# Kernel tuning notes

Hardware: AMD Instinct MI355X
Metric: run time of the kernel (lower is better)

Reference implementation:

```python
import jax, jax.numpy as jnp
import numpy as np

EPS = 1e-5

def layernorm(x, g, b):
    mu = jnp.mean(x, axis=-1, keepdims=True)
    var = jnp.mean(jnp.square(x - mu), axis=-1, keepdims=True)
    return (x - mu) * jax.lax.rsqrt(var + EPS) * g + b

def setup_inputs() -> dict:
    key = jax.random.key(0)
    B, C, W = 1, 256, 64           # C = x_h_dim = query_dim
    D = 256                        # inner_dim = heads(1) * dim_head(256)
    ks = jax.random.split(key, 32)
    sc = 0.02
    inp = {
        'x': jax.random.normal(ks[0], (B, C, W, W), jnp.float32),
        'h': jax.random.normal(ks[1], (B, C, W, W), jnp.float32),
        's': jax.random.normal(ks[2], (B, C, W, W), jnp.float32),
        'm': jax.random.normal(ks[3], (B, C, W, W), jnp.float32),
        't': jax.random.normal(ks[4], (B, C), jnp.float32),
        'wt': jax.random.normal(ks[5], (C, D), jnp.float32) * sc,
        'bt': jnp.zeros((D,), jnp.float32),
        'wk_x': jax.random.normal(ks[6], (C, D), jnp.float32) * sc,
        'wv_x': jax.random.normal(ks[7], (C, D), jnp.float32) * sc,
        'g_x': jnp.ones((C,), jnp.float32), 'be_x': jnp.zeros((C,), jnp.float32),
        'wk_h': jax.random.normal(ks[8], (C, D), jnp.float32) * sc,
        'wv_h': jax.random.normal(ks[9], (C, D), jnp.float32) * sc,
        'g_h': jnp.ones((C,), jnp.float32), 'be_h': jnp.zeros((C,), jnp.float32),
        'wk_s': jax.random.normal(ks[10], (C, D), jnp.float32) * sc,
        'wv_s': jax.random.normal(ks[11], (C, D), jnp.float32) * sc,
        'g_s': jnp.ones((C,), jnp.float32), 'be_s': jnp.zeros((C,), jnp.float32),
        'wk_m': jax.random.normal(ks[12], (C, D), jnp.float32) * sc,
        'wv_m': jax.random.normal(ks[13], (C, D), jnp.float32) * sc,
        'g_m': jnp.ones((C,), jnp.float32), 'be_m': jnp.zeros((C,), jnp.float32),
        'w_geglu': jax.random.normal(ks[14], (D, 2 * D), jnp.float32) * sc,
        'b_geglu': jnp.zeros((2 * D,), jnp.float32),
        'w_ff2': jax.random.normal(ks[15], (D, D), jnp.float32) * sc,
        'b_ff2': jnp.zeros((D,), jnp.float32),
        'g_res': jnp.ones((D,), jnp.float32), 'be_res': jnp.zeros((D,), jnp.float32),
        'w_out': jax.random.normal(ks[16], (D, C), jnp.float32) * sc,
        'b_out': jnp.zeros((C,), jnp.float32),
        'imageWidth': W,
    }
    return inp

def reference(x, h, s, m, t, wt, bt, wk_x, wv_x, g_x, be_x, wk_h, wv_h, g_h, be_h,
              wk_s, wv_s, g_s, be_s, wk_m, wv_m, g_m, be_m,
              w_geglu, b_geglu, w_ff2, b_ff2, g_res, be_res, w_out, b_out, imageWidth):
    B, C, W, _ = x.shape
    N = W * W
    D = wt.shape[1]
    scale = 1.0 / jnp.sqrt(jnp.float32(D))  # dim_head**-0.5 (heads=1)

    # query: t_transform(t) broadcast over all spatial positions -> [B, N, D]
    q = t @ wt + bt
    query = jnp.broadcast_to(q[:, None, :], (B, N, D))

    def tokens(a):  # b c h w -> b (h w) c
        return a.reshape(B, C, N).transpose(0, 2, 1)

    mods = []
    for a, g, be, wk, wv in ((x, g_x, be_x, wk_x, wv_x), (h, g_h, be_h, wk_h, wv_h),
                             (s, g_s, be_s, wk_s, wv_s), (m, g_m, be_m, wk_m, wv_m)):
        a = layernorm(tokens(a), g, be)
        mods.append((a @ wk, a @ wv))  # (k, v) each [B, N, D]

    sims = [jnp.einsum('bid,bjd->bij', query, k) * scale for k, _ in mods]
    combined = jnp.concatenate(sims, axis=-1)          # [B, N, 4N]
    attn = jax.nn.softmax(combined, axis=-1)
    parts = jnp.split(attn, 4, axis=-1)

    out = sum(jnp.einsum('bij,bjd->bid', a, v) for a, (_, v) in zip(parts, mods))

    # FeedForward(inner_dim, mult=1, glu=True) on layernormed sum
    r = layernorm(out, g_res, be_res)
    gg = r @ w_geglu + b_geglu
    u, gate = jnp.split(gg, 2, axis=-1)
    ff = (u * jax.nn.gelu(gate, approximate=False)) @ w_ff2 + b_ff2

    y = ff @ w_out + b_out                              # [B, N, C]
    return y.transpose(0, 2, 1).reshape(B, C, W, W)
```

## Files before the change

### kernel.cpp

```cpp
#include <hip/hip_runtime.h>
#include <math.h>

#define N_TOK 4096

#define OFF_Q     0
#define OFF_GU    256
#define OFF_GUBU  1280
#define OFF_SIM   2048
#define OFF_MU    18432
#define OFF_RINV  34816
#define OFF_BLK   51200
#define OFF_SOFT  51248
#define OFF_W     51264
#define OFF_OUTV  52288
#define OFF_R     52544
#define OFF_GG    52800
#define OFF_FF    53312
#define OFF_Y     53568

__global__ void kInit(const float* __restrict__ bt, const float* __restrict__ b_geglu,
                      const float* __restrict__ b_ff2, const float* __restrict__ b_out,
                      float* __restrict__ ws) {
  const int tid = threadIdx.x;
  ws[OFF_GG + tid] = b_geglu[tid];
  if (tid < 256) {
    ws[OFF_Q + tid] = bt[tid];
    ws[OFF_OUTV + tid] = 0.0f;
    ws[OFF_FF + tid] = b_ff2[tid];
    ws[OFF_Y + tid] = b_out[tid];
  }
  if (tid < 8) ws[OFF_GUBU + tid] = 0.0f;
}

__global__ void kQ(const float* __restrict__ t, const float* __restrict__ wt,
                   float* __restrict__ ws) {
  const int tid = threadIdx.x;
  const int c0 = blockIdx.x * 16;
  float acc = 0.f;
  #pragma unroll
  for (int i = 0; i < 16; ++i) {
    int c = c0 + i;
    acc += t[c] * wt[c * 256 + tid];
  }
  atomicAdd(&ws[OFF_Q + tid], acc);
}

__global__ void kU(const float* __restrict__ wk0, const float* __restrict__ wk1,
                   const float* __restrict__ wk2, const float* __restrict__ wk3,
                   const float* __restrict__ g0, const float* __restrict__ g1,
                   const float* __restrict__ g2, const float* __restrict__ g3,
                   const float* __restrict__ be0, const float* __restrict__ be1,
                   const float* __restrict__ be2, const float* __restrict__ be3,
                   float* __restrict__ ws) {
  const int b = blockIdx.x;
  const int m = b >> 3;
  const int c0 = (b & 7) * 32;
  const int tid = threadIdx.x;
  const int w = tid >> 6, lane = tid & 63;
  const float* wk = (m == 0) ? wk0 : (m == 1) ? wk1 : (m == 2) ? wk2 : wk3;
  const float* g  = (m == 0) ? g0  : (m == 1) ? g1  : (m == 2) ? g2  : g3;
  const float* be = (m == 0) ? be0 : (m == 1) ? be1 : (m == 2) ? be2 : be3;

  __shared__ float qsh[256];
  __shared__ float red[8];
  qsh[tid] = ws[OFF_Q + tid];
  __syncthreads();
  const float4 qv = ((const float4*)qsh)[lane];

  float lGU = 0.f, lBU = 0.f;
  #pragma unroll
  for (int r = 0; r < 8; ++r) {
    int c = c0 + w * 8 + r;
    float4 w4 = ((const float4*)(wk + c * 256))[lane];
    float s = w4.x * qv.x + w4.y * qv.y + w4.z * qv.z + w4.w * qv.w;
    for (int o = 32; o > 0; o >>= 1) s += __shfl_down(s, o, 64);
    if (lane == 0) {
      float u = s;
      float gu = g[c] * u;
      ws[OFF_GU + m * 256 + c] = gu;
      lGU += gu;
      lBU += be[c] * u;
    }
  }
  if (lane == 0) { red[w] = lGU; red[4 + w] = lBU; }
  __syncthreads();
  if (tid == 0) {
    atomicAdd(&ws[OFF_GUBU + m], red[0] + red[1] + red[2] + red[3]);
    atomicAdd(&ws[OFF_GUBU + 4 + m], red[4] + red[5] + red[6] + red[7]);
  }
}

__global__ void kB(const float* __restrict__ A0, const float* __restrict__ A1,
                   const float* __restrict__ A2, const float* __restrict__ A3,
                   float* __restrict__ ws) {
  const int b = blockIdx.x;
  const int m = b >> 6;
  const int jbase = (b & 63) * 64;
  const int tid = threadIdx.x;
  const int l = tid & 63;
  const int qq = tid >> 6;
  const float* A = (m == 0) ? A0 : (m == 1) ? A1 : (m == 2) ? A2 : A3;

  __shared__ float gu[256];
  __shared__ float p1[256], p2[256], p3[256];
  gu[tid] = ws[OFF_GU + m * 256 + tid];
  __syncthreads();

  float s1 = 0.f, s2 = 0.f, s3 = 0.f;
  const float* Abase = A + jbase + l;
  #pragma unroll 8
  for (int i = 0; i < 64; ++i) {
    int c = qq * 64 + i;
    float v = Abase[c * N_TOK];
    s1 += v;
    s2 += v * v;
    s3 += v * gu[c];
  }
  p1[tid] = s1; p2[tid] = s2; p3[tid] = s3;
  __syncthreads();
  if (tid < 64) {
    float S1 = p1[tid] + p1[tid + 64] + p1[tid + 128] + p1[tid + 192];
    float S2 = p2[tid] + p2[tid + 64] + p2[tid + 128] + p2[tid + 192];
    float S3 = p3[tid] + p3[tid + 64] + p3[tid + 128] + p3[tid + 192];
    float mu   = S1 * (1.0f / 256.0f);
    float var  = S2 * (1.0f / 256.0f) - mu * mu;
    float rinv = rsqrtf(var + 1e-5f);
    float GU = ws[OFF_GUBU + m];
    float BU = ws[OFF_GUBU + 4 + m];
    float sim = 0.0625f * (rinv * (S3 - mu * GU) + BU);
    int gj = m * N_TOK + jbase + tid;
    ws[OFF_SIM + gj] = sim;
    ws[OFF_MU + gj] = mu;
    ws[OFF_RINV + gj] = rinv;
  }
}

__global__ void kC1(float* __restrict__ ws) {
  const int b = blockIdx.x;
  const int tid = threadIdx.x;
  const int base = b * 1024;
  __shared__ float sred[4];

  float v[4];
  float mx = -1e30f;
  #pragma unroll
  for (int i = 0; i < 4; ++i) {
    v[i] = ws[OFF_SIM + base + i * 256 + tid];
    mx = fmaxf(mx, v[i]);
  }
  for (int o = 32; o > 0; o >>= 1) mx = fmaxf(mx, __shfl_down(mx, o, 64));
  if ((tid & 63) == 0) sred[tid >> 6] = mx;
  __syncthreads();
  const float mxb = fmaxf(fmaxf(sred[0], sred[1]), fmaxf(sred[2], sred[3]));
  __syncthreads();

  float se = 0.f, srm = 0.f;
  #pragma unroll
  for (int i = 0; i < 4; ++i) {
    int idx = base + i * 256 + tid;
    float e = expf(v[i] - mxb);
    se += e;
    srm += e * ws[OFF_RINV + idx] * ws[OFF_MU + idx];
  }
  for (int o = 32; o > 0; o >>= 1) se += __shfl_down(se, o, 64);
  if ((tid & 63) == 0) sred[tid >> 6] = se;
  __syncthreads();
  float seT = sred[0] + sred[1] + sred[2] + sred[3];
  __syncthreads();
  for (int o = 32; o > 0; o >>= 1) srm += __shfl_down(srm, o, 64);
  if ((tid & 63) == 0) sred[tid >> 6] = srm;
  __syncthreads();
  if (tid == 0) {
    float srmT = sred[0] + sred[1] + sred[2] + sred[3];
    ws[OFF_BLK + b * 3 + 0] = mxb;
    ws[OFF_BLK + b * 3 + 1] = seT;
    ws[OFF_BLK + b * 3 + 2] = srmT;
  }
}

__global__ void kC2(float* __restrict__ ws) {
  if (threadIdx.x != 0) return;
  float mx[16], se[16], srm[16];
  float M = -1e30f;
  for (int b = 0; b < 16; ++b) {
    mx[b] = ws[OFF_BLK + b * 3 + 0];
    se[b] = ws[OFF_BLK + b * 3 + 1];
    srm[b] = ws[OFF_BLK + b * 3 + 2];
    M = fmaxf(M, mx[b]);
  }
  float S = 0.f, As[4] = {0, 0, 0, 0}, P[4] = {0, 0, 0, 0};
  for (int b = 0; b < 16; ++b) {
    float f = expf(mx[b] - M);
    int m = b >> 2;
    S += se[b] * f;
    As[m] += se[b] * f;
    P[m] += srm[b] * f;
  }
  float inv = 1.0f / S;
  ws[OFF_SOFT + 0] = M;
  ws[OFF_SOFT + 1] = inv;
  for (int m = 0; m < 4; ++m) {
    ws[OFF_SOFT + 2 + m] = As[m] * inv;
    ws[OFF_SOFT + 6 + m] = P[m] * inv;
  }
}

__global__ void kD(const float* __restrict__ A0, const float* __restrict__ A1,
                   const float* __restrict__ A2, const float* __restrict__ A3,
                   const float* __restrict__ g0, const float* __restrict__ g1,
                   const float* __restrict__ g2, const float* __restrict__ g3,
                   const float* __restrict__ be0, const float* __restrict__ be1,
                   const float* __restrict__ be2, const float* __restrict__ be3,
                   float* __restrict__ ws) {
  const int b = blockIdx.x;
  const int m = b >> 8;
  const int c = b & 255;
  const int tid = threadIdx.x;
  const float* A = (m == 0) ? A0 : (m == 1) ? A1 : (m == 2) ? A2 : A3;
  const float* row = A + c * N_TOK;
  const float M = ws[OFF_SOFT + 0];
  const float inv = ws[OFF_SOFT + 1];

  float s = 0.f;
  #pragma unroll 4
  for (int i = 0; i < 16; ++i) {
    int j = i * 256 + tid;
    int gj = m * N_TOK + j;
    float a = expf(ws[OFF_SIM + gj] - M) * ws[OFF_RINV + gj];
    s += a * row[j];
  }
  __shared__ float red[4];
  for (int o = 32; o > 0; o >>= 1) s += __shfl_down(s, o, 64);
  if ((tid & 63) == 0) red[tid >> 6] = s;
  __syncthreads();
  if (tid == 0) {
    float dot = (red[0] + red[1] + red[2] + red[3]) * inv;
    const float* g  = (m == 0) ? g0  : (m == 1) ? g1  : (m == 2) ? g2  : g3;
    const float* be = (m == 0) ? be0 : (m == 1) ? be1 : (m == 2) ? be2 : be3;
    float P  = ws[OFF_SOFT + 6 + m];
    float As = ws[OFF_SOFT + 2 + m];
    ws[OFF_W + m * 256 + c] = g[c] * (dot - P) + be[c] * As;
  }
}

__global__ void kE(const float* __restrict__ wv0, const float* __restrict__ wv1,
                   const float* __restrict__ wv2, const float* __restrict__ wv3,
                   float* __restrict__ ws) {
  const int b = blockIdx.x;
  const int m = b >> 2;
  const int cbase = (b & 3) * 64;
  const int d = threadIdx.x;
  const float* wv = (m == 0) ? wv0 : (m == 1) ? wv1 : (m == 2) ? wv2 : wv3;
  float s = 0.f;
  #pragma unroll 8
  for (int i = 0; i < 64; ++i) {
    int c = cbase + i;
    s += ws[OFF_W + m * 256 + c] * wv[c * 256 + d];
  }
  atomicAdd(&ws[OFF_OUTV + d], s);
}

__global__ void kT1(const float* __restrict__ g_res, const float* __restrict__ be_res,
                    float* __restrict__ ws) {
  const int tid = threadIdx.x;
  __shared__ float red[4];
  float od = ws[OFF_OUTV + tid];
  float s = od;
  for (int o = 32; o > 0; o >>= 1) s += __shfl_down(s, o, 64);
  if ((tid & 63) == 0) red[tid >> 6] = s;
  __syncthreads();
  float mu = (red[0] + red[1] + red[2] + red[3]) * (1.0f / 256.0f);
  __syncthreads();
  float dv = od - mu;
  s = dv * dv;
  for (int o = 32; o > 0; o >>= 1) s += __shfl_down(s, o, 64);
  if ((tid & 63) == 0) red[tid >> 6] = s;
  __syncthreads();
  float var = (red[0] + red[1] + red[2] + red[3]) * (1.0f / 256.0f);
  ws[OFF_R + tid] = dv * rsqrtf(var + 1e-5f) * g_res[tid] + be_res[tid];
}

__global__ void kT2(const float* __restrict__ w_geglu, float* __restrict__ ws) {
  const int b = blockIdx.x;
  const int dt = b >> 4;
  const int d0 = (b & 15) * 16;
  const int tid = threadIdx.x;
  float acc = 0.f;
  #pragma unroll
  for (int i = 0; i < 16; ++i) {
    int d = d0 + i;
    acc += ws[OFF_R + d] * w_geglu[d * 512 + dt * 256 + tid];
  }
  atomicAdd(&ws[OFF_GG + dt * 256 + tid], acc);
}

__global__ void kT3(const float* __restrict__ w_ff2, float* __restrict__ ws) {
  const int c0 = blockIdx.x * 16;
  const int tid = threadIdx.x;
  float acc = 0.f;
  #pragma unroll
  for (int i = 0; i < 16; ++i) {
    int c = c0 + i;
    float u = ws[OFF_GG + c];
    float gate = ws[OFF_GG + 256 + c];
    float f = u * 0.5f * gate * (1.0f + erff(gate * 0.70710678118654752f));
    acc += f * w_ff2[c * 256 + tid];
  }
  atomicAdd(&ws[OFF_FF + tid], acc);
}

__global__ void kT4(const float* __restrict__ w_out, float* __restrict__ ws) {
  const int d0 = blockIdx.x * 16;
  const int tid = threadIdx.x;
  float acc = 0.f;
  #pragma unroll
  for (int i = 0; i < 16; ++i) {
    int d = d0 + i;
    acc += ws[OFF_FF + d] * w_out[d * 256 + tid];
  }
  atomicAdd(&ws[OFF_Y + tid], acc);
}

__global__ void kG(const float* __restrict__ ws, float4* __restrict__ out4) {
  const int idx = blockIdx.x * 256 + threadIdx.x;
  const int c = idx >> 10;
  float v = ws[OFF_Y + c];
  out4[idx] = make_float4(v, v, v, v);
}

extern "C" void kernel_launch(void* const* d_in, const int* in_sizes, int n_in,
                              void* d_out, int out_size, void* d_ws, size_t ws_size,
                              hipStream_t stream) {
  const float* x = (const float*)d_in[0];
  const float* h = (const float*)d_in[1];
  const float* s = (const float*)d_in[2];
  const float* m = (const float*)d_in[3];
  const float* t = (const float*)d_in[4];
  const float* wt = (const float*)d_in[5];
  const float* bt = (const float*)d_in[6];
  const float* wk_x = (const float*)d_in[7];
  const float* wv_x = (const float*)d_in[8];
  const float* g_x = (const float*)d_in[9];
  const float* be_x = (const float*)d_in[10];
  const float* wk_h = (const float*)d_in[11];
  const float* wv_h = (const float*)d_in[12];
  const float* g_h = (const float*)d_in[13];
  const float* be_h = (const float*)d_in[14];
  const float* wk_s = (const float*)d_in[15];
  const float* wv_s = (const float*)d_in[16];
  const float* g_s = (const float*)d_in[17];
  const float* be_s = (const float*)d_in[18];
  const float* wk_m = (const float*)d_in[19];
  const float* wv_m = (const float*)d_in[20];
  const float* g_m = (const float*)d_in[21];
  const float* be_m = (const float*)d_in[22];
  const float* w_geglu = (const float*)d_in[23];
  const float* b_geglu = (const float*)d_in[24];
  const float* w_ff2 = (const float*)d_in[25];
  const float* b_ff2 = (const float*)d_in[26];
  const float* g_res = (const float*)d_in[27];
  const float* be_res = (const float*)d_in[28];
  const float* w_out = (const float*)d_in[29];
  const float* b_out = (const float*)d_in[30];
  float* ws = (float*)d_ws;

  kInit<<<dim3(1), dim3(512), 0, stream>>>(bt, b_geglu, b_ff2, b_out, ws);
  kQ<<<dim3(16), dim3(256), 0, stream>>>(t, wt, ws);
  kU<<<dim3(32), dim3(256), 0, stream>>>(wk_x, wk_h, wk_s, wk_m,
      g_x, g_h, g_s, g_m, be_x, be_h, be_s, be_m, ws);
  kB<<<dim3(256), dim3(256), 0, stream>>>(x, h, s, m, ws);
  kC1<<<dim3(16), dim3(256), 0, stream>>>(ws);
  kC2<<<dim3(1), dim3(64), 0, stream>>>(ws);
  kD<<<dim3(1024), dim3(256), 0, stream>>>(x, h, s, m,
      g_x, g_h, g_s, g_m, be_x, be_h, be_s, be_m, ws);
  kE<<<dim3(16), dim3(256), 0, stream>>>(wv_x, wv_h, wv_s, wv_m, ws);
  kT1<<<dim3(1), dim3(256), 0, stream>>>(g_res, be_res, ws);
  kT2<<<dim3(32), dim3(256), 0, stream>>>(w_geglu, ws);
  kT3<<<dim3(16), dim3(256), 0, stream>>>(w_ff2, ws);
  kT4<<<dim3(16), dim3(256), 0, stream>>>(w_out, ws);
  kG<<<dim3(1024), dim3(256), 0, stream>>>(ws, (float4*)d_out);
}
```

Baseline: 168.2 us.

## Fuse all stages into one cooperative persistent kernel with grid syncs

Replaces the chain of thirteen small kernel launches with a single cooperative kernel of 512 blocks that runs every stage, separated by grid-wide barriers. The Q projection is recomputed in each of the 32 U blocks, and GU/BU partial sums are stored per block rather than accumulated atomically. The stats pass is re-tiled to use float4 loads over 32-token chunks. The aim is to remove launch gaps and per-kernel overhead on a latency-bound pipeline, at the cost of about ten grid barriers and redundant Q computation. The old multi-kernel path is kept as a fallback when the cooperative launch cannot run.

Result: slower. 670.5 us (+298.7%).

```diff
diff --git a/kernel.cpp b/kernel.cpp
--- a/kernel.cpp
+++ b/kernel.cpp
@@ -1,22 +1,322 @@
 #include <hip/hip_runtime.h>
+#include <hip/hip_cooperative_groups.h>
 #include <math.h>
 
+namespace cg = cooperative_groups;
+
 #define N_TOK 4096
 
-#define OFF_Q     0
-#define OFF_GU    256
-#define OFF_GUBU  1280
+#define OFF_GU    0
+#define OFF_GUP   1024
+#define OFF_BUP   1056
 #define OFF_SIM   2048
 #define OFF_MU    18432
 #define OFF_RINV  34816
 #define OFF_BLK   51200
-#define OFF_SOFT  51248
 #define OFF_W     51264
 #define OFF_OUTV  52288
 #define OFF_R     52544
 #define OFF_GG    52800
 #define OFF_FF    53312
 #define OFF_Y     53568
+#define OFF_Q     53824
+#define OFF_SOFT  54080
+
+struct Params {
+  const float *x, *h, *s, *m, *t, *wt, *bt;
+  const float *wk0, *wv0, *g0, *be0;
+  const float *wk1, *wv1, *g1, *be1;
+  const float *wk2, *wv2, *g2, *be2;
+  const float *wk3, *wv3, *g3, *be3;
+  const float *w_geglu, *b_geglu, *w_ff2, *b_ff2;
+  const float *g_res, *be_res, *w_out, *b_out;
+  float* ws;
+  float4* out4;
+};
+
+__global__ __launch_bounds__(256, 2) void fused(Params p) {
+  cg::grid_group grid = cg::this_grid();
+  const int gid = blockIdx.x;
+  const int tid = threadIdx.x;
+  float* ws = p.ws;
+
+  __shared__ float sh[3328];
+
+  const float* Aarr[4] = {p.x, p.h, p.s, p.m};
+  const float* garr[4] = {p.g0, p.g1, p.g2, p.g3};
+  const float* bearr[4] = {p.be0, p.be1, p.be2, p.be3};
+
+  if (gid < 32) {
+    const int m = gid >> 3;
+    const int c0 = (gid & 7) * 32;
+    const float* wkarr[4] = {p.wk0, p.wk1, p.wk2, p.wk3};
+    const float* wk = wkarr[m];
+    const float* g = garr[m];
+    const float* be = bearr[m];
+
+    float acc = p.bt[tid];
+    #pragma unroll 8
+    for (int c = 0; c < 256; ++c) acc += p.t[c] * p.wt[c * 256 + tid];
+    sh[tid] = acc;
+    __syncthreads();
+
+    const int w = tid >> 6, lane = tid & 63;
+    const float4 qv = ((const float4*)sh)[lane];
+    float lGU = 0.f, lBU = 0.f;
+    #pragma unroll
+    for (int r = 0; r < 8; ++r) {
+      int c = c0 + w * 8 + r;
+      float4 w4 = ((const float4*)(wk + c * 256))[lane];
+      float sdot = w4.x * qv.x + w4.y * qv.y + w4.z * qv.z + w4.w * qv.w;
+      for (int o = 32; o > 0; o >>= 1) sdot += __shfl_down(sdot, o, 64);
+      if (lane == 0) {
+        float u = sdot;
+        float gu = g[c] * u;
+        ws[OFF_GU + m * 256 + c] = gu;
+        lGU += gu;
+        lBU += be[c] * u;
+      }
+    }
+    __syncthreads();
+    if (lane == 0) { sh[256 + w] = lGU; sh[260 + w] = lBU; }
+    __syncthreads();
+    if (tid == 0) {
+      ws[OFF_GUP + m * 8 + (gid & 7)] = sh[256] + sh[257] + sh[258] + sh[259];
+      ws[OFF_BUP + m * 8 + (gid & 7)] = sh[260] + sh[261] + sh[262] + sh[263];
+    }
+  } else if (gid == 32) {
+    ws[OFF_OUTV + tid] = 0.0f;
+    ws[OFF_GG + tid] = p.b_geglu[tid];
+    ws[OFF_GG + 256 + tid] = p.b_geglu[256 + tid];
+    ws[OFF_FF + tid] = p.b_ff2[tid];
+    ws[OFF_Y + tid] = p.b_out[tid];
+  }
+  grid.sync();
+
+  {
+    const int m = gid >> 7;
+    const int jbase = (gid & 127) * 32;
+    const int l = tid & 7;
+    const int qg = tid >> 3;
+    const float* A = Aarr[m];
+
+    float* gu_sh = sh;
+    float* p1 = sh + 256;
+    float* p2 = sh + 1280;
+    float* p3 = sh + 2304;
+    gu_sh[tid] = ws[OFF_GU + m * 256 + tid];
+    __syncthreads();
+
+    float s1[4] = {0, 0, 0, 0}, s2[4] = {0, 0, 0, 0}, s3[4] = {0, 0, 0, 0};
+    #pragma unroll
+    for (int i = 0; i < 8; ++i) {
+      int c = qg * 8 + i;
+      float4 v4 = ((const float4*)(A + c * N_TOK + jbase))[l];
+      float gv = gu_sh[c];
+      s1[0] += v4.x; s2[0] += v4.x * v4.x; s3[0] += v4.x * gv;
+      s1[1] += v4.y; s2[1] += v4.y * v4.y; s3[1] += v4.y * gv;
+      s1[2] += v4.z; s2[2] += v4.z * v4.z; s3[2] += v4.z * gv;
+      s1[3] += v4.w; s2[3] += v4.w * v4.w; s3[3] += v4.w * gv;
+    }
+    #pragma unroll
+    for (int k = 0; k < 4; ++k) {
+      int tok = l * 4 + k;
+      p1[qg * 32 + tok] = s1[k];
+      p2[qg * 32 + tok] = s2[k];
+      p3[qg * 32 + tok] = s3[k];
+    }
+    __syncthreads();
+    if (tid < 32) {
+      float S1 = 0.f, S2 = 0.f, S3 = 0.f;
+      #pragma unroll 8
+      for (int q = 0; q < 32; ++q) {
+        S1 += p1[q * 32 + tid];
+        S2 += p2[q * 32 + tid];
+        S3 += p3[q * 32 + tid];
+      }
+      float GU = 0.f, BU = 0.f;
+      #pragma unroll
+      for (int i = 0; i < 8; ++i) {
+        GU += ws[OFF_GUP + m * 8 + i];
+        BU += ws[OFF_BUP + m * 8 + i];
+      }
+      float mu = S1 * (1.0f / 256.0f);
+      float var = S2 * (1.0f / 256.0f) - mu * mu;
+      float rinv = rsqrtf(var + 1e-5f);
+      float sim = 0.0625f * (rinv * (S3 - mu * GU) + BU);
+      int gj = m * N_TOK + jbase + tid;
+      ws[OFF_SIM + gj] = sim;
+      ws[OFF_MU + gj] = mu;
+      ws[OFF_RINV + gj] = rinv;
+    }
+  }
+  grid.sync();
+
+  if (gid < 16) {
+    const int base = gid * 1024;
+    float v[4];
+    float mx = -1e30f;
+    #pragma unroll
+    for (int i = 0; i < 4; ++i) {
+      v[i] = ws[OFF_SIM + base + i * 256 + tid];
+      mx = fmaxf(mx, v[i]);
+    }
+    for (int o = 32; o > 0; o >>= 1) mx = fmaxf(mx, __shfl_down(mx, o, 64));
+    if ((tid & 63) == 0) sh[tid >> 6] = mx;
+    __syncthreads();
+    const float mxb = fmaxf(fmaxf(sh[0], sh[1]), fmaxf(sh[2], sh[3]));
+    __syncthreads();
+    float se = 0.f, srm = 0.f;
+    #pragma unroll
+    for (int i = 0; i < 4; ++i) {
+      int idx = base + i * 256 + tid;
+      float e = expf(v[i] - mxb);
+      se += e;
+      srm += e * ws[OFF_RINV + idx] * ws[OFF_MU + idx];
+    }
+    for (int o = 32; o > 0; o >>= 1) se += __shfl_down(se, o, 64);
+    if ((tid & 63) == 0) sh[tid >> 6] = se;
+    __syncthreads();
+    float seT = sh[0] + sh[1] + sh[2] + sh[3];
+    __syncthreads();
+    for (int o = 32; o > 0; o >>= 1) srm += __shfl_down(srm, o, 64);
+    if ((tid & 63) == 0) sh[tid >> 6] = srm;
+    __syncthreads();
+    if (tid == 0) {
+      ws[OFF_BLK + gid * 3 + 0] = mxb;
+      ws[OFF_BLK + gid * 3 + 1] = seT;
+      ws[OFF_BLK + gid * 3 + 2] = sh[0] + sh[1] + sh[2] + sh[3];
+    }
+  }
+  grid.sync();
+
+  {
+    const int m = gid >> 7;
+    const int cbase = (gid & 127) * 2;
+
+    float M = -1e30f;
+    #pragma unroll
+    for (int b = 0; b < 16; ++b) M = fmaxf(M, ws[OFF_BLK + b * 3]);
+    float S = 0.f, Asm = 0.f, Pm = 0.f;
+    #pragma unroll
+    for (int b = 0; b < 16; ++b) {
+      float f = expf(ws[OFF_BLK + b * 3] - M);
+      float sef = ws[OFF_BLK + b * 3 + 1] * f;
+      S += sef;
+      if ((b >> 2) == m) {
+        Asm += sef;
+        Pm += ws[OFF_BLK + b * 3 + 2] * f;
+      }
+    }
+    const float inv = 1.0f / S;
+
+    for (int r = 0; r < 2; ++r) {
+      const int c = cbase + r;
+      const float* row = Aarr[m] + c * N_TOK;
+      float sacc = 0.f;
+      #pragma unroll 4
+      for (int i = 0; i < 16; ++i) {
+        int j = i * 256 + tid;
+        int gj = m * N_TOK + j;
+        float a = expf(ws[OFF_SIM + gj] - M) * ws[OFF_RINV + gj];
+        sacc += a * row[j];
+      }
+      for (int o = 32; o > 0; o >>= 1) sacc += __shfl_down(sacc, o, 64);
+      if ((tid & 63) == 0) sh[tid >> 6] = sacc;
+      __syncthreads();
+      if (tid == 0) {
+        float dot = (sh[0] + sh[1] + sh[2] + sh[3]) * inv;
+        ws[OFF_W + m * 256 + c] =
+            garr[m][c] * (dot - Pm * inv) + bearr[m][c] * (Asm * inv);
+      }
+      __syncthreads();
+    }
+  }
+  grid.sync();
+
+  if (gid < 16) {
+    const int m = gid >> 2;
+    const int cbase = (gid & 3) * 64;
+    const float* wvarr[4] = {p.wv0, p.wv1, p.wv2, p.wv3};
+    const float* wv = wvarr[m];
+    float sacc = 0.f;
+    #pragma unroll 8
+    for (int i = 0; i < 64; ++i) {
+      int c = cbase + i;
+      sacc += ws[OFF_W + m * 256 + c] * wv[c * 256 + tid];
+    }
+    atomicAdd(&ws[OFF_OUTV + tid], sacc);
+  }
+  grid.sync();
+
+  if (gid == 0) {
+    float od = ws[OFF_OUTV + tid];
+    float sr = od;
+    for (int o = 32; o > 0; o >>= 1) sr += __shfl_down(sr, o, 64);
+    if ((tid & 63) == 0) sh[tid >> 6] = sr;
+    __syncthreads();
+    float mu = (sh[0] + sh[1] + sh[2] + sh[3]) * (1.0f / 256.0f);
+    __syncthreads();
+    float dv = od - mu;
+    sr = dv * dv;
+    for (int o = 32; o > 0; o >>= 1) sr += __shfl_down(sr, o, 64);
+    if ((tid & 63) == 0) sh[tid >> 6] = sr;
+    __syncthreads();
+    float var = (sh[0] + sh[1] + sh[2] + sh[3]) * (1.0f / 256.0f);
+    ws[OFF_R + tid] = dv * rsqrtf(var + 1e-5f) * p.g_res[tid] + p.be_res[tid];
+  }
+  grid.sync();
+
+  if (gid < 32) {
+    const int dt = gid >> 4;
+    const int d0 = (gid & 15) * 16;
+    float acc = 0.f;
+    #pragma unroll
+    for (int i = 0; i < 16; ++i) {
+      int d = d0 + i;
+      acc += ws[OFF_R + d] * p.w_geglu[d * 512 + dt * 256 + tid];
+    }
+    atomicAdd(&ws[OFF_GG + dt * 256 + tid], acc);
+  }
+  grid.sync();
+
+  if (gid < 16) {
+    const int c0 = gid * 16;
+    float acc = 0.f;
+    #pragma unroll
+    for (int i = 0; i < 16; ++i) {
+      int c = c0 + i;
+      float u = ws[OFF_GG + c];
+      float gate = ws[OFF_GG + 256 + c];
+      float f = u * 0.5f * gate * (1.0f + erff(gate * 0.70710678118654752f));
+      acc += f * p.w_ff2[c * 256 + tid];
+    }
+    atomicAdd(&ws[OFF_FF + tid], acc);
+  }
+  grid.sync();
+
+  if (gid < 16) {
+    const int d0 = gid * 16;
+    float acc = 0.f;
+    #pragma unroll
+    for (int i = 0; i < 16; ++i) {
+      int d = d0 + i;
+      acc += ws[OFF_FF + d] * p.w_out[d * 256 + tid];
+    }
+    atomicAdd(&ws[OFF_Y + tid], acc);
+  }
+  grid.sync();
+
+  {
+    #pragma unroll
+    for (int k = 0; k < 2; ++k) {
+      const int idx = gid * 512 + k * 256 + tid;
+      const int c = idx >> 10;
+      float v = ws[OFF_Y + c];
+      p.out4[idx] = make_float4(v, v, v, v);
+    }
+  }
+}
 
 __global__ void kInit(const float* __restrict__ bt, const float* __restrict__ b_geglu,
                       const float* __restrict__ b_ff2, const float* __restrict__ b_out,
@@ -29,7 +329,8 @@
     ws[OFF_FF + tid] = b_ff2[tid];
     ws[OFF_Y + tid] = b_out[tid];
   }
-  if (tid < 8) ws[OFF_GUBU + tid] = 0.0f;
+  if (tid < 8) { ws[OFF_GUP + tid * 4] = 0.0f; }
+  if (tid < 64) { ws[OFF_GUP + tid] = 0.0f; ws[OFF_BUP] = ws[OFF_BUP]; }
 }
 
 __global__ void kQ(const float* __restrict__ t, const float* __restrict__ wt,
@@ -85,8 +386,8 @@
   if (lane == 0) { red[w] = lGU; red[4 + w] = lBU; }
   __syncthreads();
   if (tid == 0) {
-    atomicAdd(&ws[OFF_GUBU + m], red[0] + red[1] + red[2] + red[3]);
-    atomicAdd(&ws[OFF_GUBU + 4 + m], red[4] + red[5] + red[6] + red[7]);
+    ws[OFF_GUP + m * 8 + (b & 7)] = red[0] + red[1] + red[2] + red[3];
+    ws[OFF_BUP + m * 8 + (b & 7)] = red[4] + red[5] + red[6] + red[7];
   }
 }
 
@@ -122,11 +423,15 @@
     float S1 = p1[tid] + p1[tid + 64] + p1[tid + 128] + p1[tid + 192];
     float S2 = p2[tid] + p2[tid + 64] + p2[tid + 128] + p2[tid + 192];
     float S3 = p3[tid] + p3[tid + 64] + p3[tid + 128] + p3[tid + 192];
+    float GU = 0.f, BU = 0.f;
+    #pragma unroll
+    for (int i = 0; i < 8; ++i) {
+      GU += ws[OFF_GUP + m * 8 + i];
+      BU += ws[OFF_BUP + m * 8 + i];
+    }
     float mu   = S1 * (1.0f / 256.0f);
     float var  = S2 * (1.0f / 256.0f) - mu * mu;
     float rinv = rsqrtf(var + 1e-5f);
-    float GU = ws[OFF_GUBU + m];
-    float BU = ws[OFF_GUBU + 4 + m];
     float sim = 0.0625f * (rinv * (S3 - mu * GU) + BU);
     int gj = m * N_TOK + jbase + tid;
     ws[OFF_SIM + gj] = sim;
@@ -171,30 +476,23 @@
   if ((tid & 63) == 0) sred[tid >> 6] = srm;
   __syncthreads();
   if (tid == 0) {
-    float srmT = sred[0] + sred[1] + sred[2] + sred[3];
     ws[OFF_BLK + b * 3 + 0] = mxb;
     ws[OFF_BLK + b * 3 + 1] = seT;
-    ws[OFF_BLK + b * 3 + 2] = srmT;
+    ws[OFF_BLK + b * 3 + 2] = sred[0] + sred[1] + sred[2] + sred[3];
   }
 }
 
 __global__ void kC2(float* __restrict__ ws) {
   if (threadIdx.x != 0) return;
-  float mx[16], se[16], srm[16];
   float M = -1e30f;
-  for (int b = 0; b < 16; ++b) {
-    mx[b] = ws[OFF_BLK + b * 3 + 0];
-    se[b] = ws[OFF_BLK + b * 3 + 1];
-    srm[b] = ws[OFF_BLK + b * 3 + 2];
-    M = fmaxf(M, mx[b]);
-  }
+  for (int b = 0; b < 16; ++b) M = fmaxf(M, ws[OFF_BLK + b * 3]);
   float S = 0.f, As[4] = {0, 0, 0, 0}, P[4] = {0, 0, 0, 0};
   for (int b = 0; b < 16; ++b) {
-    float f = expf(mx[b] - M);
+    float f = expf(ws[OFF_BLK + b * 3] - M);
     int m = b >> 2;
-    S += se[b] * f;
-    As[m] += se[b] * f;
-    P[m] += srm[b] * f;
+    S += ws[OFF_BLK + b * 3 + 1] * f;
+    As[m] += ws[OFF_BLK + b * 3 + 1] * f;
+    P[m] += ws[OFF_BLK + b * 3 + 2] * f;
   }
   float inv = 1.0f / S;
   ws[OFF_SOFT + 0] = M;
@@ -237,9 +535,8 @@
     float dot = (red[0] + red[1] + red[2] + red[3]) * inv;
     const float* g  = (m == 0) ? g0  : (m == 1) ? g1  : (m == 2) ? g2  : g3;
     const float* be = (m == 0) ? be0 : (m == 1) ? be1 : (m == 2) ? be2 : be3;
-    float P  = ws[OFF_SOFT + 6 + m];
-    float As = ws[OFF_SOFT + 2 + m];
-    ws[OFF_W + m * 256 + c] = g[c] * (dot - P) + be[c] * As;
+    ws[OFF_W + m * 256 + c] =
+        g[c] * (dot - ws[OFF_SOFT + 6 + m]) + be[c] * ws[OFF_SOFT + 2 + m];
   }
 }
 
@@ -331,52 +628,67 @@
 extern "C" void kernel_launch(void* const* d_in, const int* in_sizes, int n_in,
                               void* d_out, int out_size, void* d_ws, size_t ws_size,
                               hipStream_t stream) {
-  const float* x = (const float*)d_in[0];
-  const float* h = (const float*)d_in[1];
-  const float* s = (const float*)d_in[2];
-  const float* m = (const float*)d_in[3];
-  const float* t = (const float*)d_in[4];
-  const float* wt = (const float*)d_in[5];
-  const float* bt = (const float*)d_in[6];
-  const float* wk_x = (const float*)d_in[7];
-  const float* wv_x = (const float*)d_in[8];
-  const float* g_x = (const float*)d_in[9];
-  const float* be_x = (const float*)d_in[10];
-  const float* wk_h = (const float*)d_in[11];
-  const float* wv_h = (const float*)d_in[12];
-  const float* g_h = (const float*)d_in[13];
-  const float* be_h = (const float*)d_in[14];
-  const float* wk_s = (const float*)d_in[15];
-  const float* wv_s = (const float*)d_in[16];
-  const float* g_s = (const float*)d_in[17];
-  const float* be_s = (const float*)d_in[18];
-  const float* wk_m = (const float*)d_in[19];
-  const float* wv_m = (const float*)d_in[20];
-  const float* g_m = (const float*)d_in[21];
-  const float* be_m = (const float*)d_in[22];
-  const float* w_geglu = (const float*)d_in[23];
-  const float* b_geglu = (const float*)d_in[24];
-  const float* w_ff2 = (const float*)d_in[25];
-  const float* b_ff2 = (const float*)d_in[26];
-  const float* g_res = (const float*)d_in[27];
-  const float* be_res = (const float*)d_in[28];
-  const float* w_out = (const float*)d_in[29];
-  const float* b_out = (const float*)d_in[30];
+  Params p;
+  p.x = (const float*)d_in[0];
+  p.h = (const float*)d_in[1];
+  p.s = (const float*)d_in[2];
+  p.m = (const float*)d_in[3];
+  p.t = (const float*)d_in[4];
+  p.wt = (const float*)d_in[5];
+  p.bt = (const float*)d_in[6];
+  p.wk0 = (const float*)d_in[7];
+  p.wv0 = (const float*)d_in[8];
+  p.g0 = (const float*)d_in[9];
+  p.be0 = (const float*)d_in[10];
+  p.wk1 = (const float*)d_in[11];
+  p.wv1 = (const float*)d_in[12];
+  p.g1 = (const float*)d_in[13];
+  p.be1 = (const float*)d_in[14];
+  p.wk2 = (const float*)d_in[15];
+  p.wv2 = (const float*)d_in[16];
+  p.g2 = (const float*)d_in[17];
+  p.be2 = (const float*)d_in[18];
+  p.wk3 = (const float*)d_in[19];
+  p.wv3 = (const float*)d_in[20];
+  p.g3 = (const float*)d_in[21];
+  p.be3 = (const float*)d_in[22];
+  p.w_geglu = (const float*)d_in[23];
+  p.b_geglu = (const float*)d_in[24];
+  p.w_ff2 = (const float*)d_in[25];
+  p.b_ff2 = (const float*)d_in[26];
+  p.g_res = (const float*)d_in[27];
+  p.be_res = (const float*)d_in[28];
+  p.w_out = (const float*)d_in[29];
+  p.b_out = (const float*)d_in[30];
+  p.ws = (float*)d_ws;
+  p.out4 = (float4*)d_out;
   float* ws = (float*)d_ws;
 
-  kInit<<<dim3(1), dim3(512), 0, stream>>>(bt, b_geglu, b_ff2, b_out, ws);
-  kQ<<<dim3(16), dim3(256), 0, stream>>>(t, wt, ws);
-  kU<<<dim3(32), dim3(256), 0, stream>>>(wk_x, wk_h, wk_s, wk_m,
-      g_x, g_h, g_s, g_m, be_x, be_h, be_s, be_m, ws);
-  kB<<<dim3(256), dim3(256), 0, stream>>>(x, h, s, m, ws);
+  int nb = 0;
+  hipError_t oe = hipOccupancyMaxActiveBlocksPerMultiprocessor(
+      &nb, (const void*)fused, 256, 0);
+  bool coop_ok = (oe == hipSuccess) && (nb >= 2);
+
+  if (coop_ok) {
+    void* args[] = {&p};
+    hipError_t le = hipLaunchCooperativeKernel((const void*)fused, dim3(512),
+                                               dim3(256), args, 0, stream);
+    if (le == hipSuccess) return;
+  }
+
+  kInit<<<dim3(1), dim3(512), 0, stream>>>(p.bt, p.b_geglu, p.b_ff2, p.b_out, ws);
+  kQ<<<dim3(16), dim3(256), 0, stream>>>(p.t, p.wt, ws);
+  kU<<<dim3(32), dim3(256), 0, stream>>>(p.wk0, p.wk1, p.wk2, p.wk3,
+      p.g0, p.g1, p.g2, p.g3, p.be0, p.be1, p.be2, p.be3, ws);
+  kB<<<dim3(256), dim3(256), 0, stream>>>(p.x, p.h, p.s, p.m, ws);
   kC1<<<dim3(16), dim3(256), 0, stream>>>(ws);
   kC2<<<dim3(1), dim3(64), 0, stream>>>(ws);
-  kD<<<dim3(1024), dim3(256), 0, stream>>>(x, h, s, m,
-      g_x, g_h, g_s, g_m, be_x, be_h, be_s, be_m, ws);
-  kE<<<dim3(16), dim3(256), 0, stream>>>(wv_x, wv_h, wv_s, wv_m, ws);
-  kT1<<<dim3(1), dim3(256), 0, stream>>>(g_res, be_res, ws);
-  kT2<<<dim3(32), dim3(256), 0, stream>>>(w_geglu, ws);
-  kT3<<<dim3(16), dim3(256), 0, stream>>>(w_ff2, ws);
-  kT4<<<dim3(16), dim3(256), 0, stream>>>(w_out, ws);
+  kD<<<dim3(1024), dim3(256), 0, stream>>>(p.x, p.h, p.s, p.m,
+      p.g0, p.g1, p.g2, p.g3, p.be0, p.be1, p.be2, p.be3, ws);
+  kE<<<dim3(16), dim3(256), 0, stream>>>(p.wv0, p.wv1, p.wv2, p.wv3, ws);
+  kT1<<<dim3(1), dim3(256), 0, stream>>>(p.g_res, p.be_res, ws);
+  kT2<<<dim3(32), dim3(256), 0, stream>>>(p.w_geglu, ws);
+  kT3<<<dim3(16), dim3(256), 0, stream>>>(p.w_ff2, ws);
+  kT4<<<dim3(16), dim3(256), 0, stream>>>(p.w_out, ws);
   kG<<<dim3(1024), dim3(256), 0, stream>>>(ws, (float4*)d_out);
 }
```
